# Performance work log

Measured on AMD Instinct MI355X. Metric: run time of the kernel, lower is better.

Reference implementation:

```python
import jax, jax.numpy as jnp
import numpy as np

D = 4        # memory depth
K = 64       # number of locations
N = 262144   # number of time units
KAPPA = K + K * K * D


def setup_inputs() -> dict:
    key = jax.random.key(0)
    k_obs, k_beta = jax.random.split(key)
    obs = jax.random.uniform(k_obs, (N, K), dtype=jnp.float32)          # observations (dense stand-in for csr)
    beta = jax.random.uniform(k_beta, (1, KAPPA), dtype=jnp.float32)    # matches uniform_(0, 1) init
    return {"obs": obs, "beta": beta, "d": D}


def reference(obs, beta, d):
    n, k = obs.shape
    beta0 = beta[0, :k]                       # [K] base intensity
    B3 = beta[0, k:].reshape(k, k, d)         # [K, K, d]; B3[k,j,i] multiplies obs[t-d+i, j]
    # sliding windows W[t, i, j] = obs[t + i, j], t = 0..n-d-1  (window ending just before t+d)
    idx = jnp.arange(n - d)[:, None] + jnp.arange(d)[None, :]  # [T', d]
    W = obs[idx]                                               # [T', d, K]
    # lam[t, k] = beta0[k] + sum_{i,j} W[t,i,j] * B3[k,j,i]  (the kron(I_K, vec) matmul collapsed)
    lam = beta0[None, :] + jnp.einsum('tij,kji->tk', W, B3)    # [T', K]
    tgt = obs[d:]                                              # omega_t for t = d..n-1
    loglik = jnp.sum(tgt * jnp.log(lam)) - jnp.sum(lam)
    return loglik, lam
```

## Files before the change

### kernel.cpp

```cpp
#include <hip/hip_runtime.h>
#include <hip/hip_bf16.h>

#define NROWS 262144
#define KO 64
#define DW 4
#define TROWS (NROWS - DW)

#define AROWS 136
#define ACHUNKS (AROWS * 16)

using f32x4  = __attribute__((ext_vector_type(4))) float;
using bf16x8 = __attribute__((ext_vector_type(8))) __bf16;

typedef const __attribute__((address_space(1))) void* gas_ptr;
typedef __attribute__((address_space(3))) void* las_ptr;

__global__ void pack_b_kernel(const float* __restrict__ beta, __bf16* __restrict__ bpack,
                              float* __restrict__ out0) {
  int idx = blockIdx.x * 256 + threadIdx.x;
  if (idx == 0) out0[0] = 0.f;
  if (idx >= 2048) return;
  int lane = idx & 63;
  int kt = (idx >> 6) & 3;
  int cc = idx >> 8;
  int kout = kt * 16 + (lane & 15);
  int cbase = cc * 32 + 8 * (lane >> 4);
  __bf16* dst = bpack + idx * 8;
#pragma unroll
  for (int e = 0; e < 8; ++e) {
    int c = cbase + e;
    int i = c >> 6;
    int j = c & 63;
    dst[e] = (__bf16)beta[KO + (kout * KO + j) * DW + i];
  }
}

__launch_bounds__(256, 4)
__global__ void poisson_main_kernel(const float* __restrict__ obs,
                                    const float* __restrict__ beta,
                                    const __bf16* __restrict__ bpack,
                                    float* __restrict__ lam_out,
                                    float* __restrict__ loglik) {
  __shared__ float aLds[AROWS * KO];
  const int tid  = threadIdx.x;
  const int wave = tid >> 6;
  const int lane = tid & 63;
  const int lr = lane & 15;
  const int lg = lane >> 4;
  const int t0 = blockIdx.x * 128;

#pragma unroll
  for (int it = 0; it < 9; ++it) {
    int c = tid + it * 256;
    if (c < ACHUNKS) {
      int arow = c >> 4;
      int cb   = (c & 15) << 4;
      int row  = t0 + arow;
      if (row > NROWS - 1) row = NROWS - 1;
      const float* src = obs + row * KO + ((cb ^ ((arow & 7) << 4)) >> 2);
      __builtin_amdgcn_global_load_lds((gas_ptr)src,
          (las_ptr)(aLds + (it * 256 + wave * 64) * 4), 16, 0, 0);
    }
  }

  const __bf16* pB = bpack + lane * 8;
  float b0v[4];
#pragma unroll
  for (int kt = 0; kt < 4; ++kt) b0v[kt] = beta[kt * 16 + lr];

  f32x4 acc[2][4];
#pragma unroll
  for (int ts = 0; ts < 2; ++ts)
#pragma unroll
    for (int kt = 0; kt < 4; ++kt)
      acc[ts][kt] = (f32x4){0.f, 0.f, 0.f, 0.f};

  asm volatile("s_waitcnt vmcnt(0)" ::: "memory");
  __syncthreads();

  const int rowb = 32 * wave + lr;
#pragma unroll
  for (int cc = 0; cc < 8; ++cc) {
    const int i  = cc >> 1;
    const int sw = ((lr + i) & 7) << 4;
    const int cb = (cc & 1) * 128 + 32 * lg;
    bf16x8 ax[2];
#pragma unroll
    for (int ts = 0; ts < 2; ++ts) {
      const char* base = (const char*)aLds + (rowb + 16 * ts + i) * 256;
      f32x4 f0 = *reinterpret_cast<const f32x4*>(base + ((cb +  0) ^ sw));
      f32x4 f1 = *reinterpret_cast<const f32x4*>(base + ((cb + 16) ^ sw));
      bf16x8 av;
      av[0] = (__bf16)f0[0]; av[1] = (__bf16)f0[1];
      av[2] = (__bf16)f0[2]; av[3] = (__bf16)f0[3];
      av[4] = (__bf16)f1[0]; av[5] = (__bf16)f1[1];
      av[6] = (__bf16)f1[2]; av[7] = (__bf16)f1[3];
      ax[ts] = av;
    }
#pragma unroll
    for (int kt = 0; kt < 4; ++kt) {
      bf16x8 bfrag = *reinterpret_cast<const bf16x8*>(pB + (cc * 4 + kt) * 512);
      acc[0][kt] = __builtin_amdgcn_mfma_f32_16x16x32_bf16(ax[0], bfrag, acc[0][kt], 0, 0, 0);
      acc[1][kt] = __builtin_amdgcn_mfma_f32_16x16x32_bf16(ax[1], bfrag, acc[1][kt], 0, 0, 0);
    }
  }

  float part = 0.f;
#pragma unroll
  for (int ts = 0; ts < 2; ++ts)
#pragma unroll
    for (int r = 0; r < 4; ++r) {
      const int tl = 32 * wave + 16 * ts + 4 * lg + r;
      const int tg = t0 + tl;
      if (tg < TROWS) {
        const int trow = tl + DW;
        const int swt  = (trow & 7) << 4;
        const char* tb = (const char*)aLds + trow * 256;
        float* po = lam_out + tg * KO + lr;
#pragma unroll
        for (int kt = 0; kt < 4; ++kt) {
          const float lam = acc[ts][kt][r] + b0v[kt];
          po[kt * 16] = lam;
          const float tgt = *reinterpret_cast<const float*>(tb + (((kt * 16 + lr) * 4) ^ swt));
          part += tgt * __logf(lam) - lam;
        }
      }
    }

#pragma unroll
  for (int off = 32; off > 0; off >>= 1)
    part += __shfl_down(part, off, 64);

  __shared__ float wpart[4];
  if (lane == 0) wpart[wave] = part;
  __syncthreads();
  if (threadIdx.x == 0)
    atomicAdd(loglik, wpart[0] + wpart[1] + wpart[2] + wpart[3]);
}

extern "C" void kernel_launch(void* const* d_in, const int* in_sizes, int n_in,
                              void* d_out, int out_size, void* d_ws, size_t ws_size,
                              hipStream_t stream) {
  const float* obs  = (const float*)d_in[0];
  const float* beta = (const float*)d_in[1];
  float* out = (float*)d_out;

  __bf16* bpack = (__bf16*)d_ws;

  hipLaunchKernelGGL(pack_b_kernel, dim3(8), dim3(256), 0, stream, beta, bpack, out);
  hipLaunchKernelGGL(poisson_main_kernel, dim3(2048), dim3(256), 0, stream,
                     obs, beta, bpack, out + 1, out);
}
```

Before: 139.7 us.

## Make main kernel persistent over four tiles with double-buffered LDS prefetch

Each block now handles four 128-row tiles instead of one, with the grid cut to 512 blocks. The next tile's obs rows are prefetched into a second LDS buffer with global_load_lds while the current tile runs its MFMAs and epilogue. This hides load latency and spreads per-block setup and the atomic reduction over more work. In exchange LDS use doubles, occupancy drops (launch bounds 2), and there are fewer blocks to fill the GPU.

```diff
diff --git a/kernel.cpp b/kernel.cpp
--- a/kernel.cpp
+++ b/kernel.cpp
@@ -6,8 +6,8 @@
 #define DW 4
 #define TROWS (NROWS - DW)
 
-#define AROWS 136
-#define ACHUNKS (AROWS * 16)
+#define AROWS 144
+#define TPB 4
 
 using f32x4  = __attribute__((ext_vector_type(4))) float;
 using bf16x8 = __attribute__((ext_vector_type(8))) __bf16;
@@ -35,106 +35,121 @@
   }
 }
 
-__launch_bounds__(256, 4)
+__launch_bounds__(256, 2)
 __global__ void poisson_main_kernel(const float* __restrict__ obs,
                                     const float* __restrict__ beta,
                                     const __bf16* __restrict__ bpack,
                                     float* __restrict__ lam_out,
                                     float* __restrict__ loglik) {
-  __shared__ float aLds[AROWS * KO];
+  __shared__ float aLds[2][AROWS * KO];
+  __shared__ float wpart[4];
   const int tid  = threadIdx.x;
   const int wave = tid >> 6;
   const int lane = tid & 63;
   const int lr = lane & 15;
   const int lg = lane >> 4;
-  const int t0 = blockIdx.x * 128;
+  const int tb0 = blockIdx.x * (TPB * 128);
 
-#pragma unroll
-  for (int it = 0; it < 9; ++it) {
-    int c = tid + it * 256;
-    if (c < ACHUNKS) {
-      int arow = c >> 4;
-      int cb   = (c & 15) << 4;
-      int row  = t0 + arow;
-      if (row > NROWS - 1) row = NROWS - 1;
-      const float* src = obs + row * KO + ((cb ^ ((arow & 7) << 4)) >> 2);
-      __builtin_amdgcn_global_load_lds((gas_ptr)src,
-          (las_ptr)(aLds + (it * 256 + wave * 64) * 4), 16, 0, 0);
-    }
-  }
+#define STAGE(BUF, U) do {                                                    \
+    _Pragma("unroll")                                                         \
+    for (int it = 0; it < 9; ++it) {                                          \
+      int c = tid + it * 256;                                                 \
+      int arow = c >> 4;                                                      \
+      int cb = (c & 15) << 4;                                                 \
+      int row = tb0 + (U) * 128 + arow;                                       \
+      row = row < NROWS - 1 ? row : NROWS - 1;                                \
+      const float* src = obs + row * KO + ((cb ^ ((arow & 7) << 4)) >> 2);    \
+      __builtin_amdgcn_global_load_lds((gas_ptr)src,                          \
+          (las_ptr)(&aLds[BUF][0] + (it * 256 + wave * 64) * 4), 16, 0, 0);   \
+    }                                                                         \
+  } while (0)
 
   const __bf16* pB = bpack + lane * 8;
   float b0v[4];
 #pragma unroll
   for (int kt = 0; kt < 4; ++kt) b0v[kt] = beta[kt * 16 + lr];
 
-  f32x4 acc[2][4];
+  float part = 0.f;
+  STAGE(0, 0);
+
 #pragma unroll
-  for (int ts = 0; ts < 2; ++ts)
+  for (int u = 0; u < TPB; ++u) {
+    if (u < TPB - 1) {
+      STAGE((u + 1) & 1, u + 1);
+      asm volatile("s_waitcnt vmcnt(9)" ::: "memory");
+    } else {
+      asm volatile("s_waitcnt vmcnt(0)" ::: "memory");
+    }
+    __builtin_amdgcn_s_barrier();
+
+    const char* bufc = (const char*)&aLds[u & 1][0];
+    f32x4 acc[2][4];
 #pragma unroll
-    for (int kt = 0; kt < 4; ++kt)
-      acc[ts][kt] = (f32x4){0.f, 0.f, 0.f, 0.f};
+    for (int ts = 0; ts < 2; ++ts)
+#pragma unroll
+      for (int kt = 0; kt < 4; ++kt)
+        acc[ts][kt] = (f32x4){0.f, 0.f, 0.f, 0.f};
 
-  asm volatile("s_waitcnt vmcnt(0)" ::: "memory");
-  __syncthreads();
+    const int rowb = 32 * wave + lr;
+#pragma unroll
+    for (int cc = 0; cc < 8; ++cc) {
+      const int i  = cc >> 1;
+      const int sw = ((lr + i) & 7) << 4;
+      const int cb = (cc & 1) * 128 + 32 * lg;
+      bf16x8 ax[2];
+#pragma unroll
+      for (int ts = 0; ts < 2; ++ts) {
+        const char* base = bufc + (rowb + 16 * ts + i) * 256;
+        f32x4 f0 = *reinterpret_cast<const f32x4*>(base + ((cb +  0) ^ sw));
+        f32x4 f1 = *reinterpret_cast<const f32x4*>(base + ((cb + 16) ^ sw));
+        bf16x8 av;
+        av[0] = (__bf16)f0[0]; av[1] = (__bf16)f0[1];
+        av[2] = (__bf16)f0[2]; av[3] = (__bf16)f0[3];
+        av[4] = (__bf16)f1[0]; av[5] = (__bf16)f1[1];
+        av[6] = (__bf16)f1[2]; av[7] = (__bf16)f1[3];
+        ax[ts] = av;
+      }
+#pragma unroll
+      for (int kt = 0; kt < 4; ++kt) {
+        bf16x8 bfrag = *reinterpret_cast<const bf16x8*>(pB + (cc * 4 + kt) * 512);
+        acc[0][kt] = __builtin_amdgcn_mfma_f32_16x16x32_bf16(ax[0], bfrag, acc[0][kt], 0, 0, 0);
+        acc[1][kt] = __builtin_amdgcn_mfma_f32_16x16x32_bf16(ax[1], bfrag, acc[1][kt], 0, 0, 0);
+      }
+    }
 
-  const int rowb = 32 * wave + lr;
+    const int t0 = tb0 + u * 128;
 #pragma unroll
-  for (int cc = 0; cc < 8; ++cc) {
-    const int i  = cc >> 1;
-    const int sw = ((lr + i) & 7) << 4;
-    const int cb = (cc & 1) * 128 + 32 * lg;
-    bf16x8 ax[2];
+    for (int ts = 0; ts < 2; ++ts)
 #pragma unroll
-    for (int ts = 0; ts < 2; ++ts) {
-      const char* base = (const char*)aLds + (rowb + 16 * ts + i) * 256;
-      f32x4 f0 = *reinterpret_cast<const f32x4*>(base + ((cb +  0) ^ sw));
-      f32x4 f1 = *reinterpret_cast<const f32x4*>(base + ((cb + 16) ^ sw));
-      bf16x8 av;
-      av[0] = (__bf16)f0[0]; av[1] = (__bf16)f0[1];
-      av[2] = (__bf16)f0[2]; av[3] = (__bf16)f0[3];
-      av[4] = (__bf16)f1[0]; av[5] = (__bf16)f1[1];
-      av[6] = (__bf16)f1[2]; av[7] = (__bf16)f1[3];
-      ax[ts] = av;
-    }
+      for (int r = 0; r < 4; ++r) {
+        const int tl = 32 * wave + 16 * ts + 4 * lg + r;
+        const int tg = t0 + tl;
+        if (tg < TROWS) {
+          const int trow = tl + DW;
+          const int swt  = (trow & 7) << 4;
+          const char* tb = bufc + trow * 256;
+          float* po = lam_out + tg * KO + lr;
 #pragma unroll
-    for (int kt = 0; kt < 4; ++kt) {
-      bf16x8 bfrag = *reinterpret_cast<const bf16x8*>(pB + (cc * 4 + kt) * 512);
-      acc[0][kt] = __builtin_amdgcn_mfma_f32_16x16x32_bf16(ax[0], bfrag, acc[0][kt], 0, 0, 0);
-      acc[1][kt] = __builtin_amdgcn_mfma_f32_16x16x32_bf16(ax[1], bfrag, acc[1][kt], 0, 0, 0);
-    }
-  }
-
-  float part = 0.f;
-#pragma unroll
-  for (int ts = 0; ts < 2; ++ts)
-#pragma unroll
-    for (int r = 0; r < 4; ++r) {
-      const int tl = 32 * wave + 16 * ts + 4 * lg + r;
-      const int tg = t0 + tl;
-      if (tg < TROWS) {
-        const int trow = tl + DW;
-        const int swt  = (trow & 7) << 4;
-        const char* tb = (const char*)aLds + trow * 256;
-        float* po = lam_out + tg * KO + lr;
-#pragma unroll
-        for (int kt = 0; kt < 4; ++kt) {
-          const float lam = acc[ts][kt][r] + b0v[kt];
-          po[kt * 16] = lam;
-          const float tgt = *reinterpret_cast<const float*>(tb + (((kt * 16 + lr) * 4) ^ swt));
-          part += tgt * __logf(lam) - lam;
+          for (int kt = 0; kt < 4; ++kt) {
+            const float lam = acc[ts][kt][r] + b0v[kt];
+            po[kt * 16] = lam;
+            const float tgt = *reinterpret_cast<const float*>(tb + (((kt * 16 + lr) * 4) ^ swt));
+            part += tgt * __logf(lam) - lam;
+          }
         }
       }
-    }
+
+    __builtin_amdgcn_s_barrier();
+  }
+#undef STAGE
 
 #pragma unroll
   for (int off = 32; off > 0; off >>= 1)
     part += __shfl_down(part, off, 64);
 
-  __shared__ float wpart[4];
   if (lane == 0) wpart[wave] = part;
   __syncthreads();
-  if (threadIdx.x == 0)
+  if (tid == 0)
     atomicAdd(loglik, wpart[0] + wpart[1] + wpart[2] + wpart[3]);
 }
 
@@ -148,6 +163,6 @@
   __bf16* bpack = (__bf16*)d_ws;
 
   hipLaunchKernelGGL(pack_b_kernel, dim3(8), dim3(256), 0, stream, beta, bpack, out);
-  hipLaunchKernelGGL(poisson_main_kernel, dim3(2048), dim3(256), 0, stream,
+  hipLaunchKernelGGL(poisson_main_kernel, dim3(512), dim3(256), 0, stream,
                      obs, beta, bpack, out + 1, out);
 }
```

After: 134.5 us. -3.7%, faster.
